# Kernel tuning notes

Measured on AMD Instinct MI355X. Metric: run time of the kernel, lower is better.

## Reference

```python
import jax, jax.numpy as jnp
import numpy as np

DG = 8   # deformable_groups
KK = 9   # 3x3 kernel
NEG_SLOPE = 0.2


def conv3x3(x, w, b):
    y = jax.lax.conv_general_dilated(x, w, (1, 1), ((1, 1), (1, 1)),
                                     dimension_numbers=('NCHW', 'OIHW', 'NCHW'))
    return y + b[None, :, None, None]


def deform_sample(x, oy, ox, mask):
    # x: [B,C,H,W]; oy/ox/mask: [B,DG,KK,H,W] -> sampled [B,DG,cpg,KK,H,W]
    B, C, H, W = x.shape
    cpg = C // DG
    ky, kx = jnp.meshgrid(jnp.arange(3), jnp.arange(3), indexing='ij')
    ky = (ky.reshape(-1) - 1).astype(x.dtype)  # dilation=1, padding=1
    kx = (kx.reshape(-1) - 1).astype(x.dtype)
    hh = jnp.arange(H, dtype=x.dtype)
    ww = jnp.arange(W, dtype=x.dtype)
    py = hh[None, None, None, :, None] + ky[None, None, :, None, None] + oy
    px = ww[None, None, None, None, :] + kx[None, None, :, None, None] + ox
    y0 = jnp.floor(py)
    x0 = jnp.floor(px)
    fy = py - y0
    fx = px - x0
    xg = x.reshape(B, DG, cpg, H * W)

    def gather(yi, xi):
        valid = ((yi >= 0) & (yi < H) & (xi >= 0) & (xi < W)).astype(x.dtype)
        yc = jnp.clip(yi, 0, H - 1)
        xc = jnp.clip(xi, 0, W - 1)
        idx = (yc * W + xc).reshape(B, DG, 1, KK * H * W)
        v = jnp.take_along_axis(xg, idx, axis=3).reshape(B, DG, cpg, KK, H, W)
        return v * valid[:, :, None]

    y0i = y0.astype(jnp.int32)
    x0i = x0.astype(jnp.int32)
    v00 = gather(y0i, x0i)
    v01 = gather(y0i, x0i + 1)
    v10 = gather(y0i + 1, x0i)
    v11 = gather(y0i + 1, x0i + 1)
    wy = fy[:, :, None]
    wx = fx[:, :, None]
    val = (v00 * (1 - wy) * (1 - wx) + v01 * (1 - wy) * wx
           + v10 * wy * (1 - wx) + v11 * wy * wx)
    return val * mask[:, :, None]


def reference(x, offset, w_off, b_off, w_dcn, b_dcn, w_conv1, b_conv1):
    B, C, H, W = x.shape
    om = conv3x3(offset, w_off, b_off)  # [B, 3*DG*KK, H, W]
    o1, o2, m = jnp.split(om, 3, axis=1)
    oy = o1.reshape(B, DG, KK, H, W)
    ox = o2.reshape(B, DG, KK, H, W)
    mask = jax.nn.sigmoid(m).reshape(B, DG, KK, H, W)
    sampled = deform_sample(x, oy, ox, mask)  # [B,DG,cpg,KK,H,W]
    wd = w_dcn.reshape(w_dcn.shape[0], DG, C // DG, KK)
    dcn = jnp.einsum('bgckhw,ogck->bohw', sampled, wd) + b_dcn[None, :, None, None]
    fea = jnp.where(dcn >= 0, dcn, NEG_SLOPE * dcn)  # LeakyReLU(0.2)
    out = conv3x3(fea, w_conv1, b_conv1) + x  # residual
    return out


def setup_inputs() -> dict:
    key = jax.random.key(0)
    ks = jax.random.split(key, 8)
    B, C, H, W = 4, 64, 96, 96
    offC = 64
    s = 1.0 / np.sqrt(C * 9)
    return {
        'x': jax.random.normal(ks[0], (B, C, H, W), jnp.float32),
        'offset': jax.random.normal(ks[1], (B, offC, H, W), jnp.float32),
        'w_off': jax.random.normal(ks[2], (3 * DG * KK, offC, 3, 3), jnp.float32) * 0.05,
        'b_off': jnp.zeros((3 * DG * KK,), jnp.float32),
        'w_dcn': jax.random.normal(ks[3], (C, C, 3, 3), jnp.float32) * s,
        'b_dcn': jnp.zeros((C,), jnp.float32),
        'w_conv1': jax.random.normal(ks[4], (C, C, 3, 3), jnp.float32) * s,
        'b_conv1': jnp.zeros((C,), jnp.float32),
    }
```

## Files before the change

kernel.cpp:

```cpp
#include <hip/hip_runtime.h>
#include <math.h>

#define HH 96
#define WW 96
#define NB 4
#define NC 64
#define HW (HH*WW)
#define PH 98
#define PW 98
#define PHW (PH*PW)
#define NPP (NB*PHW)

typedef unsigned short u16;
typedef unsigned int   u32;
typedef __attribute__((ext_vector_type(8))) short bf16x8;
typedef __attribute__((ext_vector_type(4))) float f32x4;

__device__ inline float bf2f(u16 v) { u32 u = ((u32)v) << 16; return __uint_as_float(u); }
__device__ inline u16 f2bf(float f) {
    u32 u = __float_as_uint(f);
    return (u16)((u + 0x7FFFu + ((u >> 16) & 1u)) >> 16);
}
__device__ __forceinline__ float elemf(const u32* a, int i) {
    u32 v = a[i >> 1];
    v = (i & 1) ? (v & 0xFFFF0000u) : (v << 16);
    return __uint_as_float(v);
}

__global__ __launch_bounds__(256) void k_prep(
    const float* __restrict__ x, const float* __restrict__ offset,
    const float* __restrict__ w_off, const float* __restrict__ w_dcn,
    const float* __restrict__ w_c1,
    u16* __restrict__ xt, u16* __restrict__ otp, u16* __restrict__ feap,
    u16* __restrict__ d_off, u16* __restrict__ d_dcn, u16* __restrict__ d_c1) {
    int bx = blockIdx.x;
    int tid = threadIdx.x;
    if (bx < 144) {
        int pix = bx * 256 + tid;
        int b = pix / HW, hw = pix % HW;
        const float* s = x + b * 64 * HW + hw;
        uint4* dp = (uint4*)(xt + pix * 64);
#pragma unroll
        for (int q = 0; q < 8; ++q) {
            u32 a0 = (u32)f2bf(s[(q*8+0)*HW]) | ((u32)f2bf(s[(q*8+1)*HW]) << 16);
            u32 a1 = (u32)f2bf(s[(q*8+2)*HW]) | ((u32)f2bf(s[(q*8+3)*HW]) << 16);
            u32 a2 = (u32)f2bf(s[(q*8+4)*HW]) | ((u32)f2bf(s[(q*8+5)*HW]) << 16);
            u32 a3 = (u32)f2bf(s[(q*8+6)*HW]) | ((u32)f2bf(s[(q*8+7)*HW]) << 16);
            dp[q] = make_uint4(a0, a1, a2, a3);
        }
        return;
    }
    if (bx < 295) {
        int pp = (bx - 144) * 256 + tid;
        if (pp >= NPP) return;
        int bp = pp / PHW, rem = pp % PHW;
        int py = rem / PW, px = rem % PW;
        int y = py - 1, xx = px - 1;
        uint4* dp = (uint4*)(otp + (size_t)pp * 64);
        if (y >= 0 && y < HH && xx >= 0 && xx < WW) {
            const float* s = offset + bp * 64 * HW + y * WW + xx;
#pragma unroll
            for (int q = 0; q < 8; ++q) {
                u32 a0 = (u32)f2bf(s[(q*8+0)*HW]) | ((u32)f2bf(s[(q*8+1)*HW]) << 16);
                u32 a1 = (u32)f2bf(s[(q*8+2)*HW]) | ((u32)f2bf(s[(q*8+3)*HW]) << 16);
                u32 a2 = (u32)f2bf(s[(q*8+4)*HW]) | ((u32)f2bf(s[(q*8+5)*HW]) << 16);
                u32 a3 = (u32)f2bf(s[(q*8+6)*HW]) | ((u32)f2bf(s[(q*8+7)*HW]) << 16);
                dp[q] = make_uint4(a0, a1, a2, a3);
            }
        } else {
            uint4 z = make_uint4(0u, 0u, 0u, 0u);
#pragma unroll
            for (int q = 0; q < 8; ++q) dp[q] = z;
        }
        return;
    }
    if (bx < 446) {
        int pp = (bx - 295) * 256 + tid;
        if (pp >= NPP) return;
        uint4* dp = (uint4*)(feap + (size_t)pp * 64);
        uint4 z = make_uint4(0u, 0u, 0u, 0u);
#pragma unroll
        for (int q = 0; q < 8; ++q) dp[q] = z;
        return;
    }
    int rel = bx - 446;
    int m, i0;
    if (rel < 576)      { m = 0; i0 = rel * 256; }
    else if (rel < 720) { m = 1; i0 = (rel - 576) * 256; }
    else                { m = 2; i0 = (rel - 720) * 256; }
    const float* w = (m == 0) ? w_off : ((m == 1) ? w_dcn : w_c1);
    u16* dst = (m == 0) ? d_off : ((m == 1) ? d_dcn : d_c1);
    int NT   = (m == 0) ? 16 : 4;
    int NCO  = (m == 0) ? 216 : 64;
    int i = i0 + tid;
    if (i >= 18 * NT * 512) return;
    int j = i & 7, L = (i >> 3) & 63;
    int cot = (i >> 9) % NT, t = (i >> 9) / NT;
    int k = t * 32 + ((L >> 4) << 3) + j;
    int co = cot * 16 + (L & 15);
    float v = 0.f;
    if (co < NCO) {
        int ci, q;
        if (m == 1) { int c = k & 7, gk = k >> 3; int kk = gk % 9, g = gk / 9; ci = g*8+c; q = kk; }
        else        { q = k >> 6; ci = k & 63; }
        v = w[co * 576 + ci * 9 + q];
    }
    dst[i] = f2bf(v);
}

__global__ __launch_bounds__(256) void k_gemm_off(
    const u16* __restrict__ otp, const u16* __restrict__ wtb,
    const float* __restrict__ bias, u16* __restrict__ omr) {
    __shared__ __align__(16) char smem[32768];
    u16* lb = (u16*)smem;
    int tid = threadIdx.x;
    int wid = tid >> 6, L = tid & 63, lr = L & 15, lk = L >> 4;
    int pixblk = blockIdx.x * 64;
    int pixA = pixblk + wid * 16 + lr;
    int b = pixblk / HW;
    int hw = pixA % HW, y = hw / WW, x = hw % WW;
    int Abase = ((b * PH + y + 1) * PW + (x + 1)) * 64;

    f32x4 acc[14];
#pragma unroll
    for (int i = 0; i < 14; ++i) acc[i] = (f32x4){0.f, 0.f, 0.f, 0.f};

    for (int t = 0; t < 18; ++t) {
        if (t) __syncthreads();
        {
            const uint4* s = (const uint4*)(wtb + t * 8192);
            uint4* d = (uint4*)lb;
            for (int i = tid; i < 896; i += 256) d[i] = s[i];
        }
        __syncthreads();
        int q = t >> 1;
        int c0 = (t & 1) * 32 + lk * 8;
        int aoff = ((q / 3 - 1) * PW + (q % 3 - 1)) * 64 + c0;
        bf16x8 a = *(const bf16x8*)(otp + Abase + aoff);
        const u16* wp = lb + L * 8;
#pragma unroll
        for (int cot = 0; cot < 14; ++cot) {
            bf16x8 bf = *(const bf16x8*)(wp + cot * 512);
            acc[cot] = __builtin_amdgcn_mfma_f32_16x16x32_bf16(a, bf, acc[cot], 0, 0, 0);
        }
    }

    __syncthreads();
    u16* om_s = (u16*)smem;
#pragma unroll
    for (int cot = 0; cot < 14; ++cot) {
        int co = cot * 16 + lr;
        if (co < 216) {
            int cls = co / 72;
            int c   = co % 72;
            int g   = c / 9, kk = c % 9;
            int slot = g * 32 + cls * 9 + kk;
            float bs = bias[co];
#pragma unroll
            for (int r = 0; r < 4; ++r) {
                float v = acc[cot][r] + bs;
                if (cls == 2) v = 1.f / (1.f + __expf(-v));
                om_s[(wid * 16 + lk * 4 + r) * 256 + slot] = f2bf(v);
            }
        }
    }
    __syncthreads();
    {
        const uint4* s = (const uint4*)om_s;
        uint4* d = (uint4*)(omr + (size_t)pixblk * 256);
#pragma unroll
        for (int i = 0; i < 8; ++i) d[tid + i * 256] = s[tid + i * 256];
    }
}

__global__ __launch_bounds__(256) void k_sdcn(
    const u16* __restrict__ xt, const u16* __restrict__ omr,
    const u16* __restrict__ wtb, const float* __restrict__ bias,
    u16* __restrict__ feap) {
    __shared__ u16 sv[32 * 576];
    int tid = threadIdx.x;
    int pixblk = blockIdx.x * 32;
    int p = tid >> 3, g = tid & 7;
    int pix = pixblk + p;
    int b = pixblk / HW;
    int hw = pix % HW, h = hw / WW, w = hw % WW;

    {
        const u16* xb = xt + b * HW * 64 + g * 8;
        const uint4* op = (const uint4*)(omr + (size_t)pix * 256 + g * 32);
        uint4 o0 = op[0], o1 = op[1], o2 = op[2], o3 = op[3];
        u32 oa[16] = {o0.x,o0.y,o0.z,o0.w, o1.x,o1.y,o1.z,o1.w,
                      o2.x,o2.y,o2.z,o2.w, o3.x,o3.y,o3.z,o3.w};

        float pw00[2], pw01[2], pw10[2], pw11[2];
        int   pi00[2], pi01[2], pi10[2], pi11[2];
        uint4 q00[2], q01[2], q10[2], q11[2];

#define CALC(kk, s) {                                                          \
        float oy   = elemf(oa, (kk));                                          \
        float ox   = elemf(oa, 9 + (kk));                                      \
        float mask = elemf(oa, 18 + (kk));                                     \
        float py = (float)(h + (kk) / 3 - 1) + oy;                             \
        float px = (float)(w + (kk) % 3 - 1) + ox;                             \
        float y0f = floorf(py), x0f = floorf(px);                              \
        float fy = py - y0f, fx = px - x0f;                                    \
        int y0 = (int)y0f, x0 = (int)x0f, y1 = y0 + 1, x1 = x0 + 1;            \
        int yc0 = min(max(y0, 0), HH-1), yc1 = min(max(y1, 0), HH-1);          \
        int xc0 = min(max(x0, 0), WW-1), xc1 = min(max(x1, 0), WW-1);          \
        float u0 = 1.f - fy, u1 = fy, s0 = 1.f - fx, s1 = fx;                  \
        pw00[s] = (y0 >= 0 && y0 < HH && x0 >= 0 && x0 < WW) ? u0*s0*mask : 0.f; \
        pw01[s] = (y0 >= 0 && y0 < HH && x1 >= 0 && x1 < WW) ? u0*s1*mask : 0.f; \
        pw10[s] = (y1 >= 0 && y1 < HH && x0 >= 0 && x0 < WW) ? u1*s0*mask : 0.f; \
        pw11[s] = (y1 >= 0 && y1 < HH && x1 >= 0 && x1 < WW) ? u1*s1*mask : 0.f; \
        pi00[s] = yc0*WW + xc0; pi01[s] = yc0*WW + xc1;                        \
        pi10[s] = yc1*WW + xc0; pi11[s] = yc1*WW + xc1; }
#define ISSUE(s) {                                                             \
        q00[s] = *(const uint4*)(xb + pi00[s]*64);                             \
        q01[s] = *(const uint4*)(xb + pi01[s]*64);                             \
        q10[s] = *(const uint4*)(xb + pi10[s]*64);                             \
        q11[s] = *(const uint4*)(xb + pi11[s]*64); }

        CALC(0, 0); ISSUE(0);
#pragma unroll
        for (int kk = 0; kk < 9; ++kk) {
            int cur = kk & 1, nxt = cur ^ 1;
            if (kk < 8) { CALC(kk + 1, nxt); ISSUE(nxt); }
            float w00 = pw00[cur], w01 = pw01[cur], w10 = pw10[cur], w11 = pw11[cur];
            uint4 a4 = q00[cur], b4 = q01[cur], c4 = q10[cur], d4 = q11[cur];
            float r[8];
            {
                float a, bb, c, d;
                a=__uint_as_float(a4.x<<16); bb=__uint_as_float(b4.x<<16); c=__uint_as_float(c4.x<<16); d=__uint_as_float(d4.x<<16);
                r[0]=w00*a+w01*bb+w10*c+w11*d;
                a=__uint_as_float(a4.x&0xFFFF0000u); bb=__uint_as_float(b4.x&0xFFFF0000u); c=__uint_as_float(c4.x&0xFFFF0000u); d=__uint_as_float(d4.x&0xFFFF0000u);
                r[1]=w00*a+w01*bb+w10*c+w11*d;
                a=__uint_as_float(a4.y<<16); bb=__uint_as_float(b4.y<<16); c=__uint_as_float(c4.y<<16); d=__uint_as_float(d4.y<<16);
                r[2]=w00*a+w01*bb+w10*c+w11*d;
                a=__uint_as_float(a4.y&0xFFFF0000u); bb=__uint_as_float(b4.y&0xFFFF0000u); c=__uint_as_float(c4.y&0xFFFF0000u); d=__uint_as_float(d4.y&0xFFFF0000u);
                r[3]=w00*a+w01*bb+w10*c+w11*d;
                a=__uint_as_float(a4.z<<16); bb=__uint_as_float(b4.z<<16); c=__uint_as_float(c4.z<<16); d=__uint_as_float(d4.z<<16);
                r[4]=w00*a+w01*bb+w10*c+w11*d;
                a=__uint_as_float(a4.z&0xFFFF0000u); bb=__uint_as_float(b4.z&0xFFFF0000u); c=__uint_as_float(c4.z&0xFFFF0000u); d=__uint_as_float(d4.z&0xFFFF0000u);
                r[5]=w00*a+w01*bb+w10*c+w11*d;
                a=__uint_as_float(a4.w<<16); bb=__uint_as_float(b4.w<<16); c=__uint_as_float(c4.w<<16); d=__uint_as_float(d4.w<<16);
                r[6]=w00*a+w01*bb+w10*c+w11*d;
                a=__uint_as_float(a4.w&0xFFFF0000u); bb=__uint_as_float(b4.w&0xFFFF0000u); c=__uint_as_float(c4.w&0xFFFF0000u); d=__uint_as_float(d4.w&0xFFFF0000u);
                r[7]=w00*a+w01*bb+w10*c+w11*d;
            }
            u32 a0 = (u32)f2bf(r[0]) | ((u32)f2bf(r[1]) << 16);
            u32 a1 = (u32)f2bf(r[2]) | ((u32)f2bf(r[3]) << 16);
            u32 a2 = (u32)f2bf(r[4]) | ((u32)f2bf(r[5]) << 16);
            u32 a3 = (u32)f2bf(r[6]) | ((u32)f2bf(r[7]) << 16);
            int slot = g * 9 + kk;
            *(uint4*)((char*)sv + p * 1152 + ((slot * 16) ^ ((p & 7) << 4))) = make_uint4(a0, a1, a2, a3);
        }
#undef CALC
#undef ISSUE
    }
    __syncthreads();

    int wid = tid >> 6, L = tid & 63, lr = L & 15, lk = L >> 4;
    int pbase = (wid & 1) * 16, cbase = (wid >> 1) * 2;
    int arow = pbase + lr;

    f32x4 acc[2];
    acc[0] = (f32x4){0.f, 0.f, 0.f, 0.f};
    acc[1] = (f32x4){0.f, 0.f, 0.f, 0.f};
#pragma unroll
    for (int t = 0; t < 18; ++t) {
        bf16x8 a = *(const bf16x8*)((const char*)sv + arow * 1152 + (((t * 4 + lk) * 16) ^ ((arow & 7) << 4)));
#pragma unroll
        for (int ct = 0; ct < 2; ++ct) {
            bf16x8 bf = *(const bf16x8*)(wtb + ((t * 4 + cbase + ct) * 64 + L) * 8);
            acc[ct] = __builtin_amdgcn_mfma_f32_16x16x32_bf16(a, bf, acc[ct], 0, 0, 0);
        }
    }
    int hwb = pixblk % HW;
    int hb = hwb / WW, wb = hwb % WW;
#pragma unroll
    for (int ct = 0; ct < 2; ++ct) {
        int co = (cbase + ct) * 16 + lr;
        float bs = bias[co];
#pragma unroll
        for (int r = 0; r < 4; ++r) {
            float v = acc[ct][r] + bs;
            v = (v >= 0.f) ? v : 0.2f * v;
            feap[((b * PH + hb + 1) * PW + (wb + 1 + pbase + lk * 4 + r)) * 64 + co] = f2bf(v);
        }
    }
}

__global__ __launch_bounds__(256) void k_gemm_c1(
    const u16* __restrict__ feap, const u16* __restrict__ wtb,
    const float* __restrict__ bias, const float* __restrict__ xres,
    float* __restrict__ out) {
    __shared__ __align__(16) char smraw[36864];
    u16* lb = (u16*)smraw;
    int tid = threadIdx.x;
    int wid = tid >> 6, L = tid & 63, lr = L & 15, lk = L >> 4;
    int pixblk = blockIdx.x * 64;
    int pixA = pixblk + wid * 16 + lr;
    int b = pixblk / HW;
    int hw = pixA % HW, y = hw / WW, x = hw % WW;
    int Abase = ((b * PH + y + 1) * PW + (x + 1)) * 64;

    f32x4 acc[4];
#pragma unroll
    for (int i = 0; i < 4; ++i) acc[i] = (f32x4){0.f, 0.f, 0.f, 0.f};

    {
        const uint4* s = (const uint4*)wtb;
        uint4* d = (uint4*)lb;
#pragma unroll
        for (int i = 0; i < 9; ++i) d[tid + i * 256] = s[tid + i * 256];
    }
    __syncthreads();
    for (int half = 0; half < 2; ++half) {
        int tbase = half * 9;
#pragma unroll
        for (int tl = 0; tl < 9; ++tl) {
            int t = tbase + tl;
            int q = t >> 1;
            int c0 = (t & 1) * 32 + lk * 8;
            int aoff = ((q / 3 - 1) * PW + (q % 3 - 1)) * 64 + c0;
            bf16x8 a = *(const bf16x8*)(feap + Abase + aoff);
            const u16* wp = lb + (tl * 256 + L) * 8;
#pragma unroll
            for (int cot = 0; cot < 4; ++cot) {
                bf16x8 bf = *(const bf16x8*)(wp + cot * 512);
                acc[cot] = __builtin_amdgcn_mfma_f32_16x16x32_bf16(a, bf, acc[cot], 0, 0, 0);
            }
        }
        __syncthreads();
        if (half == 0) {
            const uint4* s = (const uint4*)(wtb + 18432);
            uint4* d = (uint4*)lb;
#pragma unroll
            for (int i = 0; i < 9; ++i) d[tid + i * 256] = s[tid + i * 256];
            __syncthreads();
        }
    }
    float* ob = (float*)smraw;
#pragma unroll
    for (int cot = 0; cot < 4; ++cot) {
#pragma unroll
        for (int r = 0; r < 4; ++r)
            ob[(wid * 16 + lk * 4 + r) * 66 + cot * 16 + lr] = acc[cot][r];
    }
    __syncthreads();
    int p = tid & 63, cg = tid >> 6;
    int hw0 = pixblk % HW;
#pragma unroll
    for (int i = 0; i < 16; ++i) {
        int co = cg * 16 + i;
        int idx = (b * 64 + co) * HW + hw0 + p;
        out[idx] = ob[p * 66 + co] + bias[co] + xres[idx];
    }
}

extern "C" void kernel_launch(void* const* d_in, const int* in_sizes, int n_in,
                              void* d_out, int out_size, void* d_ws, size_t ws_size,
                              hipStream_t stream) {
    const float* x       = (const float*)d_in[0];
    const float* offset  = (const float*)d_in[1];
    const float* w_off   = (const float*)d_in[2];
    const float* b_off   = (const float*)d_in[3];
    const float* w_dcn   = (const float*)d_in[4];
    const float* b_dcn   = (const float*)d_in[5];
    const float* w_conv1 = (const float*)d_in[6];
    const float* b_conv1 = (const float*)d_in[7];
    float* out = (float*)d_out;

    char* ws = (char*)d_ws;
    u16* omr     = (u16*)(ws);
    u16* xt      = (u16*)(ws + 18874368);
    u16* otp     = (u16*)(ws + 23592960);
    u16* feap    = (u16*)(ws + 28510208);
    u16* wtb_off = (u16*)(ws + 33427456);
    u16* wtb_dcn = (u16*)(ws + 33722368);
    u16* wtb_c1  = (u16*)(ws + 33796096);

    hipLaunchKernelGGL(k_prep, dim3(1310), dim3(256), 0, stream,
                       x, offset, w_off, w_dcn, w_conv1, xt, otp, feap,
                       wtb_off, wtb_dcn, wtb_c1);
    hipLaunchKernelGGL(k_gemm_off, dim3(576), dim3(256), 0, stream, otp, wtb_off, b_off, omr);
    hipLaunchKernelGGL(k_sdcn, dim3(1152), dim3(256), 0, stream, xt, omr, wtb_dcn, b_dcn, feap);
    hipLaunchKernelGGL(k_gemm_c1, dim3(576), dim3(256), 0, stream, feap, wtb_c1, b_conv1, x, out);
}
```

Before: 161.0 us.

## Split deformable sampling taps across two thread halves with 512-thread blocks

```diff
diff --git a/kernel.cpp b/kernel.cpp
--- a/kernel.cpp
+++ b/kernel.cpp
@@ -173,14 +173,16 @@
     }
 }
 
-__global__ __launch_bounds__(256) void k_sdcn(
+__global__ __launch_bounds__(512) void k_sdcn(
     const u16* __restrict__ xt, const u16* __restrict__ omr,
     const u16* __restrict__ wtb, const float* __restrict__ bias,
     u16* __restrict__ feap) {
     __shared__ u16 sv[32 * 576];
     int tid = threadIdx.x;
     int pixblk = blockIdx.x * 32;
-    int p = tid >> 3, g = tid & 7;
+    int half = tid >> 8;
+    int t8 = tid & 255;
+    int p = t8 >> 3, g = t8 & 7;
     int pix = pixblk + p;
     int b = pixblk / HW;
     int hw = pix % HW, h = hw / WW, w = hw % WW;
@@ -192,11 +194,7 @@
         u32 oa[16] = {o0.x,o0.y,o0.z,o0.w, o1.x,o1.y,o1.z,o1.w,
                       o2.x,o2.y,o2.z,o2.w, o3.x,o3.y,o3.z,o3.w};
 
-        float pw00[2], pw01[2], pw10[2], pw11[2];
-        int   pi00[2], pi01[2], pi10[2], pi11[2];
-        uint4 q00[2], q01[2], q10[2], q11[2];
-
-#define CALC(kk, s) {                                                          \
+#define TAP(kk) {                                                              \
         float oy   = elemf(oa, (kk));                                          \
         float ox   = elemf(oa, 9 + (kk));                                      \
         float mask = elemf(oa, 18 + (kk));                                     \
@@ -208,85 +206,67 @@
         int yc0 = min(max(y0, 0), HH-1), yc1 = min(max(y1, 0), HH-1);          \
         int xc0 = min(max(x0, 0), WW-1), xc1 = min(max(x1, 0), WW-1);          \
         float u0 = 1.f - fy, u1 = fy, s0 = 1.f - fx, s1 = fx;                  \
-        pw00[s] = (y0 >= 0 && y0 < HH && x0 >= 0 && x0 < WW) ? u0*s0*mask : 0.f; \
-        pw01[s] = (y0 >= 0 && y0 < HH && x1 >= 0 && x1 < WW) ? u0*s1*mask : 0.f; \
-        pw10[s] = (y1 >= 0 && y1 < HH && x0 >= 0 && x0 < WW) ? u1*s0*mask : 0.f; \
-        pw11[s] = (y1 >= 0 && y1 < HH && x1 >= 0 && x1 < WW) ? u1*s1*mask : 0.f; \
-        pi00[s] = yc0*WW + xc0; pi01[s] = yc0*WW + xc1;                        \
-        pi10[s] = yc1*WW + xc0; pi11[s] = yc1*WW + xc1; }
-#define ISSUE(s) {                                                             \
-        q00[s] = *(const uint4*)(xb + pi00[s]*64);                             \
-        q01[s] = *(const uint4*)(xb + pi01[s]*64);                             \
-        q10[s] = *(const uint4*)(xb + pi10[s]*64);                             \
-        q11[s] = *(const uint4*)(xb + pi11[s]*64); }
-
-        CALC(0, 0); ISSUE(0);
-#pragma unroll
-        for (int kk = 0; kk < 9; ++kk) {
-            int cur = kk & 1, nxt = cur ^ 1;
-            if (kk < 8) { CALC(kk + 1, nxt); ISSUE(nxt); }
-            float w00 = pw00[cur], w01 = pw01[cur], w10 = pw10[cur], w11 = pw11[cur];
-            uint4 a4 = q00[cur], b4 = q01[cur], c4 = q10[cur], d4 = q11[cur];
-            float r[8];
-            {
-                float a, bb, c, d;
-                a=__uint_as_float(a4.x<<16); bb=__uint_as_float(b4.x<<16); c=__uint_as_float(c4.x<<16); d=__uint_as_float(d4.x<<16);
-                r[0]=w00*a+w01*bb+w10*c+w11*d;
-                a=__uint_as_float(a4.x&0xFFFF0000u); bb=__uint_as_float(b4.x&0xFFFF0000u); c=__uint_as_float(c4.x&0xFFFF0000u); d=__uint_as_float(d4.x&0xFFFF0000u);
-                r[1]=w00*a+w01*bb+w10*c+w11*d;
-                a=__uint_as_float(a4.y<<16); bb=__uint_as_float(b4.y<<16); c=__uint_as_float(c4.y<<16); d=__uint_as_float(d4.y<<16);
-                r[2]=w00*a+w01*bb+w10*c+w11*d;
-                a=__uint_as_float(a4.y&0xFFFF0000u); bb=__uint_as_float(b4.y&0xFFFF0000u); c=__uint_as_float(c4.y&0xFFFF0000u); d=__uint_as_float(d4.y&0xFFFF0000u);
-                r[3]=w00*a+w01*bb+w10*c+w11*d;
-                a=__uint_as_float(a4.z<<16); bb=__uint_as_float(b4.z<<16); c=__uint_as_float(c4.z<<16); d=__uint_as_float(d4.z<<16);
-                r[4]=w00*a+w01*bb+w10*c+w11*d;
-                a=__uint_as_float(a4.z&0xFFFF0000u); bb=__uint_as_float(b4.z&0xFFFF0000u); c=__uint_as_float(c4.z&0xFFFF0000u); d=__uint_as_float(d4.z&0xFFFF0000u);
-                r[5]=w00*a+w01*bb+w10*c+w11*d;
-                a=__uint_as_float(a4.w<<16); bb=__uint_as_float(b4.w<<16); c=__uint_as_float(c4.w<<16); d=__uint_as_float(d4.w<<16);
-                r[6]=w00*a+w01*bb+w10*c+w11*d;
-                a=__uint_as_float(a4.w&0xFFFF0000u); bb=__uint_as_float(b4.w&0xFFFF0000u); c=__uint_as_float(c4.w&0xFFFF0000u); d=__uint_as_float(d4.w&0xFFFF0000u);
-                r[7]=w00*a+w01*bb+w10*c+w11*d;
-            }
-            u32 a0 = (u32)f2bf(r[0]) | ((u32)f2bf(r[1]) << 16);
-            u32 a1 = (u32)f2bf(r[2]) | ((u32)f2bf(r[3]) << 16);
-            u32 a2 = (u32)f2bf(r[4]) | ((u32)f2bf(r[5]) << 16);
-            u32 a3 = (u32)f2bf(r[6]) | ((u32)f2bf(r[7]) << 16);
-            int slot = g * 9 + kk;
-            *(uint4*)((char*)sv + p * 1152 + ((slot * 16) ^ ((p & 7) << 4))) = make_uint4(a0, a1, a2, a3);
-        }
-#undef CALC
-#undef ISSUE
+        float w00 = (y0 >= 0 && y0 < HH && x0 >= 0 && x0 < WW) ? u0*s0*mask : 0.f; \
+        float w01 = (y0 >= 0 && y0 < HH && x1 >= 0 && x1 < WW) ? u0*s1*mask : 0.f; \
+        float w10 = (y1 >= 0 && y1 < HH && x0 >= 0 && x0 < WW) ? u1*s0*mask : 0.f; \
+        float w11 = (y1 >= 0 && y1 < HH && x1 >= 0 && x1 < WW) ? u1*s1*mask : 0.f; \
+        uint4 a4 = *(const uint4*)(xb + (yc0*WW + xc0)*64);                    \
+        uint4 b4 = *(const uint4*)(xb + (yc0*WW + xc1)*64);                    \
+        uint4 c4 = *(const uint4*)(xb + (yc1*WW + xc0)*64);                    \
+        uint4 d4 = *(const uint4*)(xb + (yc1*WW + xc1)*64);                    \
+        float r[8];                                                            \
+        {                                                                      \
+            float a, bb, c, d;                                                 \
+            a=__uint_as_float(a4.x<<16); bb=__uint_as_float(b4.x<<16); c=__uint_as_float(c4.x<<16); d=__uint_as_float(d4.x<<16); \
+            r[0]=w00*a+w01*bb+w10*c+w11*d;                                     \
+            a=__uint_as_float(a4.x&0xFFFF0000u); bb=__uint_as_float(b4.x&0xFFFF0000u); c=__uint_as_float(c4.x&0xFFFF0000u); d=__uint_as_float(d4.x&0xFFFF0000u); \
+            r[1]=w00*a+w01*bb+w10*c+w11*d;                                     \
+            a=__uint_as_float(a4.y<<16); bb=__uint_as_float(b4.y<<16); c=__uint_as_float(c4.y<<16); d=__uint_as_float(d4.y<<16); \
+            r[2]=w00*a+w01*bb+w10*c+w11*d;                                     \
+            a=__uint_as_float(a4.y&0xFFFF0000u); bb=__uint_as_float(b4.y&0xFFFF0000u); c=__uint_as_float(c4.y&0xFFFF0000u); d=__uint_as_float(d4.y&0xFFFF0000u); \
+            r[3]=w00*a+w01*bb+w10*c+w11*d;                                     \
+            a=__uint_as_float(a4.z<<16); bb=__uint_as_float(b4.z<<16); c=__uint_as_float(c4.z<<16); d=__uint_as_float(d4.z<<16); \
+            r[4]=w00*a+w01*bb+w10*c+w11*d;                                     \
+            a=__uint_as_float(a4.z&0xFFFF0000u); bb=__uint_as_float(b4.z&0xFFFF0000u); c=__uint_as_float(c4.z&0xFFFF0000u); d=__uint_as_float(d4.z&0xFFFF0000u); \
+            r[5]=w00*a+w01*bb+w10*c+w11*d;                                     \
+            a=__uint_as_float(a4.w<<16); bb=__uint_as_float(b4.w<<16); c=__uint_as_float(c4.w<<16); d=__uint_as_float(d4.w<<16); \
+            r[6]=w00*a+w01*bb+w10*c+w11*d;                                     \
+            a=__uint_as_float(a4.w&0xFFFF0000u); bb=__uint_as_float(b4.w&0xFFFF0000u); c=__uint_as_float(c4.w&0xFFFF0000u); d=__uint_as_float(d4.w&0xFFFF0000u); \
+            r[7]=w00*a+w01*bb+w10*c+w11*d;                                     \
+        }                                                                      \
+        u32 q0 = (u32)f2bf(r[0]) | ((u32)f2bf(r[1]) << 16);                    \
+        u32 q1 = (u32)f2bf(r[2]) | ((u32)f2bf(r[3]) << 16);                    \
+        u32 q2 = (u32)f2bf(r[4]) | ((u32)f2bf(r[5]) << 16);                    \
+        u32 q3 = (u32)f2bf(r[6]) | ((u32)f2bf(r[7]) << 16);                    \
+        int slot = g * 9 + (kk);                                               \
+        *(uint4*)((char*)sv + p * 1152 + ((slot * 16) ^ ((p & 7) << 4))) = make_uint4(q0, q1, q2, q3); }
+
+        if (half == 0) { TAP(0); TAP(1); TAP(2); TAP(3); TAP(4); }
+        else           { TAP(5); TAP(6); TAP(7); TAP(8); }
+#undef TAP
     }
     __syncthreads();
 
     int wid = tid >> 6, L = tid & 63, lr = L & 15, lk = L >> 4;
-    int pbase = (wid & 1) * 16, cbase = (wid >> 1) * 2;
-    int arow = pbase + lr;
-
-    f32x4 acc[2];
-    acc[0] = (f32x4){0.f, 0.f, 0.f, 0.f};
-    acc[1] = (f32x4){0.f, 0.f, 0.f, 0.f};
+    int mh = wid & 1, cot = wid >> 1;
+    int arow = mh * 16 + lr;
+
+    f32x4 acc = (f32x4){0.f, 0.f, 0.f, 0.f};
 #pragma unroll
     for (int t = 0; t < 18; ++t) {
         bf16x8 a = *(const bf16x8*)((const char*)sv + arow * 1152 + (((t * 4 + lk) * 16) ^ ((arow & 7) << 4)));
-#pragma unroll
-        for (int ct = 0; ct < 2; ++ct) {
-            bf16x8 bf = *(const bf16x8*)(wtb + ((t * 4 + cbase + ct) * 64 + L) * 8);
-            acc[ct] = __builtin_amdgcn_mfma_f32_16x16x32_bf16(a, bf, acc[ct], 0, 0, 0);
-        }
+        bf16x8 bf = *(const bf16x8*)(wtb + ((t * 4 + cot) * 64 + L) * 8);
+        acc = __builtin_amdgcn_mfma_f32_16x16x32_bf16(a, bf, acc, 0, 0, 0);
     }
     int hwb = pixblk % HW;
     int hb = hwb / WW, wb = hwb % WW;
-#pragma unroll
-    for (int ct = 0; ct < 2; ++ct) {
-        int co = (cbase + ct) * 16 + lr;
-        float bs = bias[co];
-#pragma unroll
-        for (int r = 0; r < 4; ++r) {
-            float v = acc[ct][r] + bs;
-            v = (v >= 0.f) ? v : 0.2f * v;
-            feap[((b * PH + hb + 1) * PW + (wb + 1 + pbase + lk * 4 + r)) * 64 + co] = f2bf(v);
-        }
+    int co = cot * 16 + lr;
+    float bs = bias[co];
+#pragma unroll
+    for (int r = 0; r < 4; ++r) {
+        float v = acc[r] + bs;
+        v = (v >= 0.f) ? v : 0.2f * v;
+        feap[((b * PH + hb + 1) * PW + (wb + 1 + mh * 16 + lk * 4 + r)) * 64 + co] = f2bf(v);
     }
 }
 
@@ -384,6 +364,6 @@
                        x, offset, w_off, w_dcn, w_conv1, xt, otp, feap,
                        wtb_off, wtb_dcn, wtb_c1);
     hipLaunchKernelGGL(k_gemm_off, dim3(576), dim3(256), 0, stream, otp, wtb_off, b_off, omr);
-    hipLaunchKernelGGL(k_sdcn, dim3(1152), dim3(256), 0, stream, xt, omr, wtb_dcn, b_dcn, feap);
+    hipLaunchKernelGGL(k_sdcn, dim3(1152), dim3(512), 0, stream, xt, omr, wtb_dcn, b_dcn, feap);
     hipLaunchKernelGGL(k_gemm_c1, dim3(576), dim3(256), 0, stream, feap, wtb_c1, b_conv1, x, out);
 }
```

After: 161.8 us. Within noise of the previous version (+0.5%).
